# Kernel optimization log

Hardware: AMD Instinct MI355X
Metric: run time of the kernel (lower is better)

The kernel has to match this reference:

```python
import jax, jax.numpy as jnp
import numpy as np

HIDDEN = 1024
HEADS = 16
HEAD_DIM = HIDDEN // HEADS


def setup_inputs() -> dict:
    key = jax.random.key(0)
    ks = jax.random.split(key, 9)
    B, S = 2, 2048
    std = 1.0 / np.sqrt(HIDDEN)
    def lin(k):
        return jax.random.uniform(k, (HIDDEN, HIDDEN), jnp.float32, -std, std)
    def bias(k):
        return jax.random.uniform(k, (HIDDEN,), jnp.float32, -std, std)
    return {
        "x": jax.random.normal(ks[0], (B, S, HIDDEN), jnp.float32),
        "Wq": lin(ks[1]), "bq": bias(ks[2]),
        "Wk": lin(ks[3]), "bk": bias(ks[4]),
        "Wv": lin(ks[5]), "bv": bias(ks[6]),
        "Wo": lin(ks[7]), "bo": bias(ks[8]),
    }


def reference(x, Wq, bq, Wk, bk, Wv, bv, Wo, bo):
    B, S, _ = x.shape
    scale = HEAD_DIM ** -0.5
    # projections; weights stored as (in, out) so y = x @ W + b
    def split_heads(y):
        return y.reshape(B, S, HEADS, HEAD_DIM).transpose(0, 2, 1, 3)  # b h s d
    q = split_heads(x @ Wq + bq)
    k = split_heads(x @ Wk + bk)
    v = split_heads(x @ Wv + bv)
    # dense attention: full [B,H,S,S] score matrix, as in the original
    scores = jnp.einsum("bhsd,bhtd->bhst", q, k) * scale
    attn = jax.nn.softmax(scores, axis=-1)
    out = jnp.einsum("bhst,bhtd->bhsd", attn, v)
    out = out.transpose(0, 2, 1, 3).reshape(B, S, HIDDEN)
    return out @ Wo + bo
```

## Files before the change

kernel.cpp:

```cpp
#include <hip/hip_runtime.h>
#include <hip/hip_bf16.h>

typedef unsigned short u16;
typedef __bf16 bf16x8 __attribute__((ext_vector_type(8)));
typedef float f32x4 __attribute__((ext_vector_type(4)));

#define HIDDEN 1024
#define NH 16
#define HD 64
#define BATCH 2
#define SEQ 2048
#define MTOT (BATCH*SEQ)
#define CEXP 0.18033688f

__device__ __forceinline__ u16 f2bf(float f) {
  union { float f; unsigned u; } v; v.f = f;
  unsigned u = v.u;
  return (u16)((u + 0x7fffu + ((u >> 16) & 1u)) >> 16);
}

__device__ __forceinline__ unsigned pack2bf(float a, float b) {
  __hip_bfloat162 h = __float22bfloat162_rn(make_float2(a, b));
  unsigned u; __builtin_memcpy(&u, &h, 4); return u;
}

__device__ __forceinline__ void gload16(const u16* g, u16* l) {
  __builtin_amdgcn_global_load_lds((const __attribute__((address_space(1))) unsigned int*)g,
                                   (__attribute__((address_space(3))) unsigned int*)l, 16, 0, 0);
}

__global__ __launch_bounds__(256) void convert_x_kernel(const float* __restrict__ x,
                                                        u16* __restrict__ xb) {
  size_t i = ((size_t)blockIdx.x * 256 + threadIdx.x) * 4;
  float4 v = *(const float4*)(x + i);
  uint2 p;
  p.x = pack2bf(v.x, v.y);
  p.y = pack2bf(v.z, v.w);
  *(uint2*)(xb + i) = p;
}

__global__ __launch_bounds__(256) void transpose_w_kernel(const float* __restrict__ w0, const float* __restrict__ w1,
                                                          const float* __restrict__ w2, const float* __restrict__ w3,
                                                          u16* __restrict__ dqkv, u16* __restrict__ dwo) {
  __shared__ float t[32][33];
  int z = blockIdx.z;
  const float* src = (z==0) ? w0 : (z==1) ? w1 : (z==2) ? w2 : w3;
  u16* dst = (z < 3) ? (dqkv + (size_t)z * HIDDEN * HIDDEN) : dwo;
  int kb = blockIdx.x * 32, nb = blockIdx.y * 32;
  int tx = threadIdx.x & 31, ty = threadIdx.x >> 5;
  for (int r = ty; r < 32; r += 8) t[r][tx] = src[(size_t)(kb + r) * HIDDEN + nb + tx];
  __syncthreads();
  for (int r = ty; r < 32; r += 8) dst[(size_t)(nb + r) * HIDDEN + kb + tx] = f2bf(t[tx][r]);
}

__global__ __launch_bounds__(256) void transpose_v_kernel(const u16* __restrict__ qkv,
                                                          u16* __restrict__ vt) {
  __shared__ u16 t[32][33];
  int bh = blockIdx.z; int b = bh >> 4, h = bh & 15;
  int t0 = blockIdx.x * 32, d0 = blockIdx.y * 32;
  int tx = threadIdx.x & 31, ty = threadIdx.x >> 5;
  for (int r = ty; r < 32; r += 8)
    t[r][tx] = qkv[(size_t)(b*SEQ + t0 + r) * (3*HIDDEN) + 2*HIDDEN + h*HD + d0 + tx];
  __syncthreads();
  for (int r = ty; r < 32; r += 8)
    vt[(size_t)(bh*HD + d0 + r) * SEQ + t0 + tx] = t[tx][r];
}

template<int MODE, int MT>
__global__ __launch_bounds__(256) void gemm_bt(const u16* __restrict__ A, const u16* __restrict__ Bt,
                                               const float* __restrict__ b0, const float* __restrict__ b1,
                                               const float* __restrict__ b2,
                                               u16* __restrict__ Cq, float* __restrict__ Cf,
                                               int M, int N, int K) {
  constexpr int MF = MT / 32;
  __shared__ u16 As[MT*32];
  __shared__ u16 Bs[128*32];
  const int tid = threadIdx.x, lane = tid & 63, wv = tid >> 6;
  const int m0 = blockIdx.x * MT, n0 = blockIdx.y * 128;
  const int wm = (wv >> 1) * (MT/2), wn = (wv & 1) * 64;
  const int col = lane & 15, quad = lane >> 4;
  const int lr = lane >> 2, lk = (lane & 3) * 8;
  f32x4 acc[MF][4] = {};
  for (int k0 = 0; k0 < K; k0 += 32) {
    if constexpr (MT == 128) {
      gload16(&A[(size_t)(m0 + wv*32      + lr)*K + k0 + lk], &As[wv*1024]);
      gload16(&A[(size_t)(m0 + wv*32 + 16 + lr)*K + k0 + lk], &As[wv*1024 + 512]);
    } else {
      gload16(&A[(size_t)(m0 + wv*16      + lr)*K + k0 + lk], &As[wv*512]);
    }
    gload16(&Bt[(size_t)(n0 + wv*32      + lr)*K + k0 + lk], &Bs[wv*1024]);
    gload16(&Bt[(size_t)(n0 + wv*32 + 16 + lr)*K + k0 + lk], &Bs[wv*1024 + 512]);
    __syncthreads();
    bf16x8 af[MF], bfr[4];
    #pragma unroll
    for (int i = 0; i < MF; i++) af[i]  = *(const bf16x8*)&As[(wm + i*16 + col)*32 + quad*8];
    #pragma unroll
    for (int i = 0; i < 4; i++)  bfr[i] = *(const bf16x8*)&Bs[(wn + i*16 + col)*32 + quad*8];
    #pragma unroll
    for (int mi = 0; mi < MF; mi++)
      #pragma unroll
      for (int ni = 0; ni < 4; ni++)
        acc[mi][ni] = __builtin_amdgcn_mfma_f32_16x16x32_bf16(af[mi], bfr[ni], acc[mi][ni], 0, 0, 0);
    __syncthreads();
  }
  if constexpr (MODE == 0) {
    #pragma unroll
    for (int mi = 0; mi < MF; mi++)
      #pragma unroll
      for (int ni = 0; ni < 4; ni++) {
        int n = n0 + wn + ni*16 + col;
        float bias = b0[n];
        #pragma unroll
        for (int r = 0; r < 4; r++) {
          int m = m0 + wm + mi*16 + quad*4 + r;
          Cf[(size_t)m*N + n] = acc[mi][ni][r] + bias;
        }
      }
  } else {
    const int seg = n0 >> 10;
    const float* bias = (seg == 0) ? b0 : (seg == 1) ? b1 : b2;
    const float scl = (seg == 0) ? CEXP : 1.0f;
    #pragma unroll
    for (int mi = 0; mi < MF; mi++)
      #pragma unroll
      for (int ni = 0; ni < 4; ni++) {
        int n = n0 + wn + ni*16 + col;
        float bv = bias[n & (HIDDEN-1)];
        #pragma unroll
        for (int r = 0; r < 4; r++) {
          int m = m0 + wm + mi*16 + quad*4 + r;
          Cq[(size_t)m*N + n] = f2bf((acc[mi][ni][r] + bv) * scl);
        }
      }
  }
}

__global__ __launch_bounds__(256) void attn_kernel(const u16* __restrict__ qkv,
                                                   const u16* __restrict__ vt,
                                                   u16* __restrict__ ao) {
  __shared__ u16 Ks[2*64*72];
  __shared__ u16 Vs[2*64*72];
  __shared__ u16 Ps[4][32*72];
  const int tid = threadIdx.x, lane = tid & 63, wv = tid >> 6;
  const int qt = blockIdx.x, bh = blockIdx.y;
  const int b = bh >> 4, h = bh & 15;
  const int col = lane & 15, quad = lane >> 4;

  bf16x8 qf[2][2];
  #pragma unroll
  for (int nq = 0; nq < 2; nq++) {
    const u16* qrow = qkv + (size_t)(b*SEQ + qt*128 + wv*32 + nq*16 + col) * (3*HIDDEN) + h*HD + quad*8;
    qf[nq][0] = *(const bf16x8*)(qrow);
    qf[nq][1] = *(const bf16x8*)(qrow + 32);
  }
  bf16x8 ones;
  #pragma unroll
  for (int i = 0; i < 8; i++) ones[i] = (__bf16)1.0f;

  f32x4 o[2][4] = {};
  f32x4 rsacc[2] = {};

  const int r0 = tid >> 3, r1 = (tid >> 3) + 32, koS = (tid & 7) * 8;
  const u16* gK = qkv + (size_t)b*SEQ*(3*HIDDEN) + HIDDEN + (size_t)h*HD;
  const u16* gV = vt + (size_t)bh*HD*SEQ;
  uint4 pK0 = *(const uint4*)&gK[(size_t)r0*(3*HIDDEN) + koS];
  uint4 pK1 = *(const uint4*)&gK[(size_t)r1*(3*HIDDEN) + koS];
  uint4 pV0 = *(const uint4*)&gV[(size_t)r0*SEQ + koS];
  uint4 pV1 = *(const uint4*)&gV[(size_t)r1*SEQ + koS];

  for (int it = 0; it < SEQ/64; ++it) {
    const int cur = (it & 1) * 4608;
    *(uint4*)&Ks[cur + r0*72 + koS] = pK0;
    *(uint4*)&Ks[cur + r1*72 + koS] = pK1;
    *(uint4*)&Vs[cur + r0*72 + koS] = pV0;
    *(uint4*)&Vs[cur + r1*72 + koS] = pV1;
    __syncthreads();
    if (it < SEQ/64 - 1) {
      int t0 = (it + 1) * 64;
      pK0 = *(const uint4*)&gK[(size_t)(t0 + r0)*(3*HIDDEN) + koS];
      pK1 = *(const uint4*)&gK[(size_t)(t0 + r1)*(3*HIDDEN) + koS];
      pV0 = *(const uint4*)&gV[(size_t)r0*SEQ + t0 + koS];
      pV1 = *(const uint4*)&gV[(size_t)r1*SEQ + t0 + koS];
    }

    f32x4 s[2][4] = {};
    #pragma unroll
    for (int kk = 0; kk < 2; kk++)
      #pragma unroll
      for (int nt = 0; nt < 4; nt++) {
        bf16x8 kf = *(const bf16x8*)&Ks[cur + (nt*16 + col)*72 + kk*32 + quad*8];
        #pragma unroll
        for (int nq = 0; nq < 2; nq++)
          s[nq][nt] = __builtin_amdgcn_mfma_f32_16x16x32_bf16(kf, qf[nq][kk], s[nq][nt], 0, 0, 0);
      }

    #pragma unroll
    for (int nq = 0; nq < 2; nq++)
      #pragma unroll
      for (int nt = 0; nt < 4; nt++) {
        float p0 = __builtin_exp2f(s[nq][nt][0]);
        float p1 = __builtin_exp2f(s[nq][nt][1]);
        float p2 = __builtin_exp2f(s[nq][nt][2]);
        float p3 = __builtin_exp2f(s[nq][nt][3]);
        uint2 w2; w2.x = pack2bf(p0, p1); w2.y = pack2bf(p2, p3);
        *(uint2*)&Ps[wv][(nq*16 + col)*72 + nt*16 + quad*4] = w2;
      }
    asm volatile("" ::: "memory");

    #pragma unroll
    for (int kk = 0; kk < 2; kk++) {
      bf16x8 pf[2];
      #pragma unroll
      for (int nq = 0; nq < 2; nq++)
        pf[nq] = *(const bf16x8*)&Ps[wv][(nq*16 + col)*72 + kk*32 + quad*8];
      #pragma unroll
      for (int mi = 0; mi < 4; mi++) {
        bf16x8 vf = *(const bf16x8*)&Vs[cur + (mi*16 + col)*72 + kk*32 + quad*8];
        #pragma unroll
        for (int nq = 0; nq < 2; nq++)
          o[nq][mi] = __builtin_amdgcn_mfma_f32_16x16x32_bf16(vf, pf[nq], o[nq][mi], 0, 0, 0);
      }
      #pragma unroll
      for (int nq = 0; nq < 2; nq++)
        rsacc[nq] = __builtin_amdgcn_mfma_f32_16x16x32_bf16(ones, pf[nq], rsacc[nq], 0, 0, 0);
    }
  }

  #pragma unroll
  for (int nq = 0; nq < 2; nq++) {
    float inv = 1.0f / rsacc[nq][0];
    u16* aop = ao + (size_t)(b*SEQ + qt*128 + wv*32 + nq*16 + col)*HIDDEN + h*HD;
    #pragma unroll
    for (int mi = 0; mi < 4; mi++) {
      uint2 w2;
      w2.x = pack2bf(o[nq][mi][0]*inv, o[nq][mi][1]*inv);
      w2.y = pack2bf(o[nq][mi][2]*inv, o[nq][mi][3]*inv);
      *(uint2*)&aop[mi*16 + quad*4] = w2;
    }
  }
}

extern "C" void kernel_launch(void* const* d_in, const int* in_sizes, int n_in,
                              void* d_out, int out_size, void* d_ws, size_t ws_size,
                              hipStream_t stream) {
  const float* x  = (const float*)d_in[0];
  const float* Wq = (const float*)d_in[1];
  const float* bq = (const float*)d_in[2];
  const float* Wk = (const float*)d_in[3];
  const float* bk = (const float*)d_in[4];
  const float* Wv = (const float*)d_in[5];
  const float* bv = (const float*)d_in[6];
  const float* Wo = (const float*)d_in[7];
  const float* bo = (const float*)d_in[8];
  float* out = (float*)d_out;

  char* w = (char*)d_ws;
  u16* xb    = (u16*)w; w += (size_t)MTOT*HIDDEN*2;
  u16* wtqkv = (u16*)w; w += (size_t)3*HIDDEN*HIDDEN*2;
  u16* wto   = (u16*)w; w += (size_t)HIDDEN*HIDDEN*2;
  u16* qkvb  = (u16*)w; w += (size_t)MTOT*3*HIDDEN*2;
  u16* vtb   = (u16*)w; w += (size_t)BATCH*NH*HD*SEQ*2;
  u16* aob   = (u16*)w; w += (size_t)MTOT*HIDDEN*2;

  convert_x_kernel<<<(MTOT*HIDDEN)/1024, 256, 0, stream>>>(x, xb);
  transpose_w_kernel<<<dim3(32, 32, 4), 256, 0, stream>>>(Wq, Wk, Wv, Wo, wtqkv, wto);
  gemm_bt<1,128><<<dim3(32, 24), 256, 0, stream>>>(xb, wtqkv, bq, bk, bv, qkvb, nullptr, MTOT, 3*HIDDEN, HIDDEN);
  transpose_v_kernel<<<dim3(SEQ/32, 2, BATCH*NH), 256, 0, stream>>>(qkvb, vtb);
  attn_kernel<<<dim3(SEQ/128, BATCH*NH), 256, 0, stream>>>(qkvb, vtb, aob);
  gemm_bt<0,64><<<dim3(64, 8), 256, 0, stream>>>(aob, wto, bo, nullptr, nullptr, nullptr, out, MTOT, HIDDEN, HIDDEN);
}
```

Before: 151.1 us.

## Switch attention to 32x32x16 MFMA and pass P via permlane32 swap

Rewrites the attention inner loop to use 32x32x16 bf16 MFMA tiles instead of 16x16x32, changing the fragment layouts for Q, K, V and the accumulators. The softmax probabilities are repacked in registers with permlane32_swap and fed straight into the PV MFMA, which removes the per-wave shared-memory staging buffer for P along with its LDS writes and reads. It also switches to the raw hardware exp2 builtin. The cost is more complex lane bookkeeping and larger per-thread accumulator vectors, which may raise register pressure.

```diff
diff --git a/kernel.cpp b/kernel.cpp
--- a/kernel.cpp
+++ b/kernel.cpp
@@ -4,6 +4,9 @@
 typedef unsigned short u16;
 typedef __bf16 bf16x8 __attribute__((ext_vector_type(8)));
 typedef float f32x4 __attribute__((ext_vector_type(4)));
+typedef float f32x16 __attribute__((ext_vector_type(16)));
+typedef unsigned u32x2 __attribute__((ext_vector_type(2)));
+typedef unsigned u32x4 __attribute__((ext_vector_type(4)));
 
 #define HIDDEN 1024
 #define NH 16
@@ -12,6 +15,12 @@
 #define SEQ 2048
 #define MTOT (BATCH*SEQ)
 #define CEXP 0.18033688f
+
+#if __has_builtin(__builtin_amdgcn_exp2f)
+#define EXP2(x) __builtin_amdgcn_exp2f(x)
+#else
+#define EXP2(x) __builtin_exp2f(x)
+#endif
 
 __device__ __forceinline__ u16 f2bf(float f) {
   union { float f; unsigned u; } v; v.f = f;
@@ -140,25 +149,23 @@
                                                    u16* __restrict__ ao) {
   __shared__ u16 Ks[2*64*72];
   __shared__ u16 Vs[2*64*72];
-  __shared__ u16 Ps[4][32*72];
   const int tid = threadIdx.x, lane = tid & 63, wv = tid >> 6;
   const int qt = blockIdx.x, bh = blockIdx.y;
   const int b = bh >> 4, h = bh & 15;
-  const int col = lane & 15, quad = lane >> 4;
-
-  bf16x8 qf[2][2];
-  #pragma unroll
-  for (int nq = 0; nq < 2; nq++) {
-    const u16* qrow = qkv + (size_t)(b*SEQ + qt*128 + wv*32 + nq*16 + col) * (3*HIDDEN) + h*HD + quad*8;
-    qf[nq][0] = *(const bf16x8*)(qrow);
-    qf[nq][1] = *(const bf16x8*)(qrow + 32);
+  const int l31 = lane & 31, hl = lane >> 5;
+
+  bf16x8 qf[4];
+  {
+    const u16* qrow = qkv + (size_t)(b*SEQ + qt*128 + wv*32 + l31)*(3*HIDDEN) + h*HD + hl*8;
+    #pragma unroll
+    for (int kk = 0; kk < 4; kk++) qf[kk] = *(const bf16x8*)(qrow + kk*16);
   }
   bf16x8 ones;
   #pragma unroll
   for (int i = 0; i < 8; i++) ones[i] = (__bf16)1.0f;
 
-  f32x4 o[2][4] = {};
-  f32x4 rsacc[2] = {};
+  f32x16 o[2] = {};
+  f32x16 rs = {};
 
   const int r0 = tid >> 3, r1 = (tid >> 3) + 32, koS = (tid & 7) * 8;
   const u16* gK = qkv + (size_t)b*SEQ*(3*HIDDEN) + HIDDEN + (size_t)h*HD;
@@ -183,61 +190,58 @@
       pV1 = *(const uint4*)&gV[(size_t)r1*SEQ + t0 + koS];
     }
 
-    f32x4 s[2][4] = {};
-    #pragma unroll
-    for (int kk = 0; kk < 2; kk++)
-      #pragma unroll
-      for (int nt = 0; nt < 4; nt++) {
-        bf16x8 kf = *(const bf16x8*)&Ks[cur + (nt*16 + col)*72 + kk*32 + quad*8];
-        #pragma unroll
-        for (int nq = 0; nq < 2; nq++)
-          s[nq][nt] = __builtin_amdgcn_mfma_f32_16x16x32_bf16(kf, qf[nq][kk], s[nq][nt], 0, 0, 0);
-      }
-
-    #pragma unroll
-    for (int nq = 0; nq < 2; nq++)
-      #pragma unroll
-      for (int nt = 0; nt < 4; nt++) {
-        float p0 = __builtin_exp2f(s[nq][nt][0]);
-        float p1 = __builtin_exp2f(s[nq][nt][1]);
-        float p2 = __builtin_exp2f(s[nq][nt][2]);
-        float p3 = __builtin_exp2f(s[nq][nt][3]);
-        uint2 w2; w2.x = pack2bf(p0, p1); w2.y = pack2bf(p2, p3);
-        *(uint2*)&Ps[wv][(nq*16 + col)*72 + nt*16 + quad*4] = w2;
-      }
-    asm volatile("" ::: "memory");
-
-    #pragma unroll
-    for (int kk = 0; kk < 2; kk++) {
-      bf16x8 pf[2];
-      #pragma unroll
-      for (int nq = 0; nq < 2; nq++)
-        pf[nq] = *(const bf16x8*)&Ps[wv][(nq*16 + col)*72 + kk*32 + quad*8];
-      #pragma unroll
-      for (int mi = 0; mi < 4; mi++) {
-        bf16x8 vf = *(const bf16x8*)&Vs[cur + (mi*16 + col)*72 + kk*32 + quad*8];
-        #pragma unroll
-        for (int nq = 0; nq < 2; nq++)
-          o[nq][mi] = __builtin_amdgcn_mfma_f32_16x16x32_bf16(vf, pf[nq], o[nq][mi], 0, 0, 0);
-      }
-      #pragma unroll
-      for (int nq = 0; nq < 2; nq++)
-        rsacc[nq] = __builtin_amdgcn_mfma_f32_16x16x32_bf16(ones, pf[nq], rsacc[nq], 0, 0, 0);
-    }
-  }
-
+    f32x16 s[2] = {};
+    #pragma unroll
+    for (int kk = 0; kk < 4; kk++) {
+      #pragma unroll
+      for (int tt = 0; tt < 2; tt++) {
+        bf16x8 kf = *(const bf16x8*)&Ks[cur + (tt*32 + l31)*72 + kk*16 + hl*8];
+        s[tt] = __builtin_amdgcn_mfma_f32_32x32x16_bf16(kf, qf[kk], s[tt], 0, 0, 0);
+      }
+    }
+
+    #pragma unroll
+    for (int tt = 0; tt < 2; tt++) {
+      unsigned w[8];
+      #pragma unroll
+      for (int j = 0; j < 8; j++) {
+        float p0 = EXP2(s[tt][2*j]);
+        float p1 = EXP2(s[tt][2*j+1]);
+        w[j] = pack2bf(p0, p1);
+      }
+      u32x2 r02 = __builtin_amdgcn_permlane32_swap(w[0], w[2], false, false);
+      u32x2 r13 = __builtin_amdgcn_permlane32_swap(w[1], w[3], false, false);
+      u32x2 r46 = __builtin_amdgcn_permlane32_swap(w[4], w[6], false, false);
+      u32x2 r57 = __builtin_amdgcn_permlane32_swap(w[5], w[7], false, false);
+      u32x4 c0, c1;
+      c0.x = r02[0]; c0.y = r13[0]; c0.z = r02[1]; c0.w = r13[1];
+      c1.x = r46[0]; c1.y = r57[0]; c1.z = r46[1]; c1.w = r57[1];
+      bf16x8 pf0 = __builtin_bit_cast(bf16x8, c0);
+      bf16x8 pf1 = __builtin_bit_cast(bf16x8, c1);
+
+      #pragma unroll
+      for (int mt = 0; mt < 2; mt++) {
+        bf16x8 vf0 = *(const bf16x8*)&Vs[cur + (mt*32 + l31)*72 + tt*32 + hl*8];
+        bf16x8 vf1 = *(const bf16x8*)&Vs[cur + (mt*32 + l31)*72 + tt*32 + 16 + hl*8];
+        o[mt] = __builtin_amdgcn_mfma_f32_32x32x16_bf16(vf0, pf0, o[mt], 0, 0, 0);
+        o[mt] = __builtin_amdgcn_mfma_f32_32x32x16_bf16(vf1, pf1, o[mt], 0, 0, 0);
+      }
+      rs = __builtin_amdgcn_mfma_f32_32x32x16_bf16(ones, pf0, rs, 0, 0, 0);
+      rs = __builtin_amdgcn_mfma_f32_32x32x16_bf16(ones, pf1, rs, 0, 0, 0);
+    }
+  }
+
+  float inv = 1.0f / rs[0];
+  u16* aop = ao + (size_t)(b*SEQ + qt*128 + wv*32 + l31)*HIDDEN + h*HD + hl*4;
   #pragma unroll
-  for (int nq = 0; nq < 2; nq++) {
-    float inv = 1.0f / rsacc[nq][0];
-    u16* aop = ao + (size_t)(b*SEQ + qt*128 + wv*32 + nq*16 + col)*HIDDEN + h*HD;
-    #pragma unroll
-    for (int mi = 0; mi < 4; mi++) {
+  for (int mt = 0; mt < 2; mt++)
+    #pragma unroll
+    for (int a4 = 0; a4 < 4; a4++) {
       uint2 w2;
-      w2.x = pack2bf(o[nq][mi][0]*inv, o[nq][mi][1]*inv);
-      w2.y = pack2bf(o[nq][mi][2]*inv, o[nq][mi][3]*inv);
-      *(uint2*)&aop[mi*16 + quad*4] = w2;
-    }
-  }
+      w2.x = pack2bf(o[mt][4*a4+0]*inv, o[mt][4*a4+1]*inv);
+      w2.y = pack2bf(o[mt][4*a4+2]*inv, o[mt][4*a4+3]*inv);
+      *(uint2*)&aop[mt*32 + 8*a4] = w2;
+    }
 }
 
 extern "C" void kernel_launch(void* const* d_in, const int* in_sizes, int n_in,
```

Measured after the change: 130.5 us. 13.6% less time.
